# Kernel tuning notes

Measured on AMD Instinct MI355X. Metric: run time of the kernel, lower is better.

Reference implementation:

```python
import jax, jax.numpy as jnp
import numpy as np

E = 128      # n_routed_experts (hardcoded in DS_CONFIG_FOR_NEMOTRON)
I = 1856     # moe_intermediate_size
K = 6        # num_experts_per_tok
H = 512      # config.hidden_size
T = 4096     # flattened tokens (batch*seq)
C = 320      # per-expert capacity; avg load = T*K/E = 192, C=320 makes drops ~impossible


def setup_inputs() -> dict:
    key = jax.random.key(0)
    k1, k2, k3, k4, k5 = jax.random.split(key, 5)
    return {
        "hidden_states": jax.random.normal(k1, (T, H), jnp.float32),
        "top_k_index": jax.random.randint(k2, (T, K), 0, E, jnp.int32),
        "top_k_weights": jax.random.uniform(k3, (T, K), jnp.float32),
        "w_gate_up": jax.random.normal(k4, (E, H, 2 * I), jnp.float32) * 0.02,
        "w_down": jax.random.normal(k5, (E, I, H), jnp.float32) * 0.02,
    }


def reference(hidden_states, top_k_index, top_k_weights, w_gate_up, w_down):
    # Grouped-GEMM formulation of the naive per-expert loop: sort the (token, k)
    # pairs by expert, pack each expert's tokens into a fixed-capacity buffer,
    # run batched gate/up/down GEMMs over all experts at once, then weighted
    # scatter-add back to token order. Same math as the torch loop.
    N = T * K
    e = top_k_index.reshape(N)                      # expert id per pair
    tok = jnp.repeat(jnp.arange(T), K)              # token id per pair
    w = top_k_weights.reshape(N)

    order = jnp.argsort(e)                          # stable sort by expert
    e_s, tok_s, w_s = e[order], tok[order], w[order]

    counts = jax.ops.segment_sum(jnp.ones((N,), jnp.int32), e, num_segments=E)
    starts = jnp.cumsum(counts) - counts            # exclusive prefix sum
    pos = jnp.arange(N) - starts[e_s]               # rank within expert
    valid = pos < C                                 # capacity guard (never trips at this load)
    slot = jnp.where(valid, e_s * C + pos, E * C)   # overflow -> dummy slot

    # Dispatch: [E*C+1, H] buffer of gathered token states (dummy row absorbs overflow)
    buf = jnp.zeros((E * C + 1, H), hidden_states.dtype).at[slot].set(hidden_states[tok_s])
    x = buf[: E * C].reshape(E, C, H)

    gu = jnp.einsum('ech,ehf->ecf', x, w_gate_up)   # [E, C, 2I]
    gate, up = jnp.split(gu, 2, axis=-1)
    inter = jax.nn.silu(gate) * up                  # [E, C, I]
    y = jnp.einsum('eci,eih->ech', inter, w_down).reshape(E * C, H)

    # Combine: gather each pair's expert output, scale by router weight, scatter-add by token
    gather_idx = jnp.where(valid, e_s * C + pos, 0)
    pair_y = y[gather_idx] * jnp.where(valid, w_s, 0.0)[:, None]
    out = jnp.zeros((T, H), hidden_states.dtype).at[tok_s].add(pair_y)
    # use_context_proj=False: context states alias the hidden states
    return (out, out)
```

## Files before the change

### kernel.cpp

```cpp
#include <hip/hip_runtime.h>
#include <hip/hip_bf16.h>
#include <stdint.h>

#define NE 128
#define NI 1856
#define NKK 6
#define NH 512
#define NT 4096
#define CAP 320
#define NPAIR (NT*NKK)
#define LD2I (2*NI)

typedef unsigned short u16;
typedef __attribute__((ext_vector_type(4))) float f32x4;
typedef __attribute__((ext_vector_type(8))) short bf16x8;
typedef __attribute__((ext_vector_type(4))) short s16x4;
typedef const void __attribute__((address_space(1)))* gas1p;
typedef void __attribute__((address_space(3)))* gas3p;

__device__ __forceinline__ short f2bf(float f) {
  union { __hip_bfloat16 h; short s; } c; c.h = __float2bfloat16(f); return c.s;
}
__device__ __forceinline__ float bf2f(short s) {
  union { float f; unsigned u; } v; v.u = ((unsigned)(u16)s) << 16; return v.f;
}

__device__ __forceinline__ int xcd_logical(int bid, int n) {
  int q = n >> 3, r = n & 7;
  int xcd = bid & 7, j = bid >> 3;
  return xcd * q + (xcd < r ? xcd : r) + j;
}

__global__ void k_route(const int* __restrict__ topk, int* __restrict__ counts,
                        int* __restrict__ slot_of_pair, int* __restrict__ pair_of_slot) {
  int n = blockIdx.x * 256 + threadIdx.x;
  if (n >= NPAIR) return;
  int e = topk[n];
  int p = atomicAdd(&counts[e], 1);
  int s = (p < CAP) ? e * CAP + p : -1;
  slot_of_pair[n] = s;
  if (s >= 0) pair_of_slot[s] = n;
}

__global__ void k_gather(const float* __restrict__ hid, const int* __restrict__ counts,
                         const int* __restrict__ pair_of_slot, u16* __restrict__ xbuf) {
  int t = threadIdx.x;
  int row = blockIdx.x * 2 + (t >> 7);
  int c = t & 127;
  int e = row / CAP, p = row % CAP;
  if (p >= counts[e]) return;
  int n = pair_of_slot[row];
  int tok = n / NKK;
  f32x4 v = *(const f32x4*)(hid + (size_t)tok * NH + c * 4);
  s16x4 o;
  o[0] = f2bf(v[0]); o[1] = f2bf(v[1]); o[2] = f2bf(v[2]); o[3] = f2bf(v[3]);
  *(s16x4*)(xbuf + (size_t)row * NH + c * 4) = o;
}

__global__ __launch_bounds__(256, 3) void k_gemm1(
    const u16* __restrict__ xbuf, const float* __restrict__ wgu,
    const int* __restrict__ counts, u16* __restrict__ inter, int e0, int nblk)
{
  __shared__ __align__(16) char lds[40960];
  int L = xcd_logical(blockIdx.x, nblk);
  int el = L / 58, nt = L % 58;
  int e = e0 + el;
  int cnt = counts[e]; if (cnt > CAP) cnt = CAP;
  int n0 = nt * 32;
  int t = threadIdx.x, w = t >> 6, l = t & 63;
  int wm = w >> 1, wc = w & 1;
  const char* abase = (const char*)(xbuf + (size_t)e * CAP * NH);

  int bc = t & 63, bkc = t >> 6;
  int gcol = (bc < 32) ? (n0 + bc) : (NI + n0 + (bc - 32));
  const float* bsrc = wgu + (size_t)e * NH * LD2I + gcol;
  float bv[8];

  int kg16 = (l >> 4) * 16;
  int bcol0 = wc * 16 + (l & 15);
  int bswz = ((bcol0 & 3) << 4);

  for (int base = 0; base < cnt; base += 256) {
    __syncthreads();

    auto stageA = [&](int buf, int kt) {
      char* dstb = lds + buf * 16384;
      #pragma unroll
      for (int i = 0; i < 4; ++i) {
        int seg = i * 4 + w;
        int o = seg * 1024 + l * 16;
        int r = o >> 6, slot = o & 63;
        int grow = base + r; if (grow > CAP - 1) grow = CAP - 1;
        const char* g = abase + (size_t)grow * (NH * 2) + kt * 64 + (slot ^ ((r & 3) << 4));
        __builtin_amdgcn_global_load_lds((gas1p)g, (gas3p)(dstb + seg * 1024), 16, 0, 0);
      }
    };
    auto loadB = [&](int kt) {
      const float* p = bsrc + (size_t)(kt * 32 + bkc * 8) * LD2I;
      #pragma unroll
      for (int j = 0; j < 8; ++j) bv[j] = p[(size_t)j * LD2I];
    };
    auto writeB = [&](int buf) {
      bf16x8 o;
      #pragma unroll
      for (int j = 0; j < 8; ++j) o[j] = f2bf(bv[j]);
      char* bb = lds + 32768 + buf * 4096;
      *(bf16x8*)(bb + bc * 64 + ((bkc * 16) ^ ((bc & 3) << 4))) = o;
    };

    f32x4 acc[2][4][2];
    #pragma unroll
    for (int m = 0; m < 2; ++m)
      #pragma unroll
      for (int f = 0; f < 4; ++f) { acc[m][f][0] = (f32x4){0,0,0,0}; acc[m][f][1] = (f32x4){0,0,0,0}; }

    loadB(0);
    stageA(0, 0);
    writeB(0);

    for (int kt = 0; kt < 16; ++kt) {
      __syncthreads();
      int cur = kt & 1, nxt = cur ^ 1;
      if (kt + 1 < 16) { loadB(kt + 1); stageA(nxt, kt + 1); }
      const char* ab = lds + cur * 16384;
      const char* bb = lds + 32768 + cur * 4096;
      bf16x8 bg = *(const bf16x8*)(bb + bcol0 * 64 + (kg16 ^ bswz));
      bf16x8 bu = *(const bf16x8*)(bb + (32 + bcol0) * 64 + (kg16 ^ bswz));
      #pragma unroll
      for (int mt = 0; mt < 2; ++mt)
        #pragma unroll
        for (int mf = 0; mf < 4; ++mf) {
          int r = mt * 128 + wm * 64 + mf * 16 + (l & 15);
          bf16x8 af = *(const bf16x8*)(ab + r * 64 + (kg16 ^ ((r & 3) << 4)));
          acc[mt][mf][0] = __builtin_amdgcn_mfma_f32_16x16x32_bf16(af, bg, acc[mt][mf][0], 0, 0, 0);
          acc[mt][mf][1] = __builtin_amdgcn_mfma_f32_16x16x32_bf16(af, bu, acc[mt][mf][1], 0, 0, 0);
        }
      if (kt + 1 < 16) writeB(nxt);
    }

    __syncthreads();

    int cl = wc * 16 + (l & 15);
    #pragma unroll
    for (int mt = 0; mt < 2; ++mt)
      #pragma unroll
      for (int mf = 0; mf < 4; ++mf) {
        f32x4 g = acc[mt][mf][0], u = acc[mt][mf][1];
        #pragma unroll
        for (int r = 0; r < 4; ++r) {
          float gv = g[r];
          float val = gv / (1.f + __expf(-gv)) * u[r];
          int rl = mt * 128 + wm * 64 + mf * 16 + (l >> 4) * 4 + r;
          *(short*)(lds + rl * 64 + ((cl * 2) ^ ((rl & 3) << 4))) = f2bf(val);
        }
      }
    __syncthreads();
    int rmax = cnt - base; if (rmax > 256) rmax = 256;
    u16* obase = inter + (size_t)(el * CAP + base) * NI + n0;
    #pragma unroll
    for (int i = 0; i < 4; ++i) {
      int task = i * 256 + t;
      int r = task >> 2, p = task & 3;
      if (r < rmax) {
        bf16x8 v = *(const bf16x8*)(lds + r * 64 + ((p * 16) ^ ((r & 3) << 4)));
        *(bf16x8*)(obase + (size_t)r * NI + p * 8) = v;
      }
    }
  }
}

__global__ __launch_bounds__(256, 3) void k_gemm2(
    const u16* __restrict__ inter, const float* __restrict__ wdn,
    const int* __restrict__ counts, u16* __restrict__ Y, int e0, int nblk)
{
  __shared__ __align__(16) char lds[40960];
  int L = xcd_logical(blockIdx.x, nblk);
  int el = L / 8, nt = L % 8;
  int e = e0 + el;
  int cnt = counts[e]; if (cnt > CAP) cnt = CAP;
  int n0 = nt * 64;
  int t = threadIdx.x, w = t >> 6, l = t & 63;
  int wm = w >> 1, wc = w & 1;
  const char* abase = (const char*)(inter + (size_t)el * CAP * NI);

  int bc = t & 63, bkc = t >> 6;
  const float* bsrc = wdn + (size_t)e * NI * NH + n0 + bc;
  float bv[8];

  int kg16 = (l >> 4) * 16;
  int bcol0 = wc * 32 + (l & 15);
  int bswz = ((bcol0 & 3) << 4);

  for (int base = 0; base < cnt; base += 256) {
    __syncthreads();

    auto stageA = [&](int buf, int kt) {
      char* dstb = lds + buf * 16384;
      #pragma unroll
      for (int i = 0; i < 4; ++i) {
        int seg = i * 4 + w;
        int o = seg * 1024 + l * 16;
        int r = o >> 6, slot = o & 63;
        int grow = base + r; if (grow > CAP - 1) grow = CAP - 1;
        const char* g = abase + (size_t)grow * (NI * 2) + kt * 64 + (slot ^ ((r & 3) << 4));
        __builtin_amdgcn_global_load_lds((gas1p)g, (gas3p)(dstb + seg * 1024), 16, 0, 0);
      }
    };
    auto loadB = [&](int kt) {
      const float* p = bsrc + (size_t)(kt * 32 + bkc * 8) * NH;
      #pragma unroll
      for (int j = 0; j < 8; ++j) bv[j] = p[(size_t)j * NH];
    };
    auto writeB = [&](int buf) {
      bf16x8 o;
      #pragma unroll
      for (int j = 0; j < 8; ++j) o[j] = f2bf(bv[j]);
      char* bb = lds + 32768 + buf * 4096;
      *(bf16x8*)(bb + bc * 64 + ((bkc * 16) ^ ((bc & 3) << 4))) = o;
    };

    f32x4 acc[2][4][2];
    #pragma unroll
    for (int m = 0; m < 2; ++m)
      #pragma unroll
      for (int f = 0; f < 4; ++f) { acc[m][f][0] = (f32x4){0,0,0,0}; acc[m][f][1] = (f32x4){0,0,0,0}; }

    loadB(0);
    stageA(0, 0);
    writeB(0);

    for (int kt = 0; kt < 58; ++kt) {
      __syncthreads();
      int cur = kt & 1, nxt = cur ^ 1;
      if (kt + 1 < 58) { loadB(kt + 1); stageA(nxt, kt + 1); }
      const char* ab = lds + cur * 16384;
      const char* bb = lds + 32768 + cur * 4096;
      bf16x8 b0 = *(const bf16x8*)(bb + bcol0 * 64 + (kg16 ^ bswz));
      bf16x8 b1 = *(const bf16x8*)(bb + (16 + bcol0) * 64 + (kg16 ^ bswz));
      #pragma unroll
      for (int mt = 0; mt < 2; ++mt)
        #pragma unroll
        for (int mf = 0; mf < 4; ++mf) {
          int r = mt * 128 + wm * 64 + mf * 16 + (l & 15);
          bf16x8 af = *(const bf16x8*)(ab + r * 64 + (kg16 ^ ((r & 3) << 4)));
          acc[mt][mf][0] = __builtin_amdgcn_mfma_f32_16x16x32_bf16(af, b0, acc[mt][mf][0], 0, 0, 0);
          acc[mt][mf][1] = __builtin_amdgcn_mfma_f32_16x16x32_bf16(af, b1, acc[mt][mf][1], 0, 0, 0);
        }
      if (kt + 1 < 58) writeB(nxt);
    }

    __syncthreads();

    #pragma unroll
    for (int mt = 0; mt < 2; ++mt)
      #pragma unroll
      for (int mf = 0; mf < 4; ++mf)
        #pragma unroll
        for (int f = 0; f < 2; ++f) {
          f32x4 a = acc[mt][mf][f];
          int cl = wc * 32 + f * 16 + (l & 15);
          #pragma unroll
          for (int r = 0; r < 4; ++r) {
            int rl = mt * 128 + wm * 64 + mf * 16 + (l >> 4) * 4 + r;
            *(short*)(lds + rl * 128 + ((cl * 2) ^ ((rl & 7) << 4))) = f2bf(a[r]);
          }
        }
    __syncthreads();
    int rmax = cnt - base; if (rmax > 256) rmax = 256;
    u16* obase = Y + (size_t)(e * CAP + base) * NH + n0;
    #pragma unroll
    for (int i = 0; i < 8; ++i) {
      int task = i * 256 + t;
      int r = task >> 3, p = task & 7;
      if (r < rmax) {
        bf16x8 v = *(const bf16x8*)(lds + r * 128 + ((p * 16) ^ ((r & 7) << 4)));
        *(bf16x8*)(obase + (size_t)r * NH + p * 8) = v;
      }
    }
  }
}

__global__ void k_combine(const int* __restrict__ slot_of_pair, const float* __restrict__ wts,
                          const u16* __restrict__ Y, float* __restrict__ out)
{
  int t = threadIdx.x;
  int tok = blockIdx.x * 2 + (t >> 7);
  int c = t & 127;
  f32x4 a = (f32x4){0.f, 0.f, 0.f, 0.f};
  #pragma unroll
  for (int k = 0; k < NKK; ++k) {
    int n = tok * NKK + k;
    int s = slot_of_pair[n];
    if (s >= 0) {
      float wv = wts[n];
      s16x4 y = *(const s16x4*)(Y + (size_t)s * NH + c * 4);
      a[0] += wv * bf2f(y[0]);
      a[1] += wv * bf2f(y[1]);
      a[2] += wv * bf2f(y[2]);
      a[3] += wv * bf2f(y[3]);
    }
  }
  *(f32x4*)(out + (size_t)tok * NH + c * 4) = a;
  *(f32x4*)(out + (size_t)(NT + tok) * NH + c * 4) = a;
}

extern "C" void kernel_launch(void* const* d_in, const int* in_sizes, int n_in,
                              void* d_out, int out_size, void* d_ws, size_t ws_size,
                              hipStream_t stream) {
  const float* hid  = (const float*)d_in[0];
  const int*   topk = (const int*)d_in[1];
  const float* wts  = (const float*)d_in[2];
  const float* wgu  = (const float*)d_in[3];
  const float* wdn  = (const float*)d_in[4];

  char* ws = (char*)d_ws;
  size_t off = 0;
  auto alloc = [&](size_t sz) { char* p = ws + off; off = (off + sz + 255) & ~(size_t)255; return p; };
  int* counts        = (int*)alloc(NE * 4);
  int* slot_of_pair  = (int*)alloc((size_t)NPAIR * 4);
  int* pair_of_slot  = (int*)alloc((size_t)NE * CAP * 4);
  u16* xbuf          = (u16*)alloc((size_t)NE * CAP * NH * 2);
  u16* Y             = (u16*)alloc((size_t)NE * CAP * NH * 2);
  size_t remain = ws_size > off ? ws_size - off : 0;
  size_t per_e = (size_t)CAP * NI * 2;
  int chunkE = (int)(remain / per_e);
  if (chunkE > NE) chunkE = NE;
  if (chunkE < 1) chunkE = 1;
  u16* inter = (u16*)(ws + off);

  hipMemsetAsync(counts, 0, NE * 4, stream);
  k_route<<<NPAIR / 256, 256, 0, stream>>>(topk, counts, slot_of_pair, pair_of_slot);
  k_gather<<<NE * CAP / 2, 256, 0, stream>>>(hid, counts, pair_of_slot, xbuf);
  for (int e0 = 0; e0 < NE; e0 += chunkE) {
    int ce = NE - e0 < chunkE ? NE - e0 : chunkE;
    int nb1 = ce * 58;
    int nb2 = ce * 8;
    k_gemm1<<<nb1, 256, 0, stream>>>(xbuf, wgu, counts, inter, e0, nb1);
    k_gemm2<<<nb2, 256, 0, stream>>>(inter, wdn, counts, Y, e0, nb2);
  }
  k_combine<<<NT / 2, 256, 0, stream>>>(slot_of_pair, wts, Y, (float*)d_out);
}
```

Measured before the change: 642.5 us.

## Stage fp32 weights via async LDS loads with triple-buffered pipeline

Both GEMM kernels now copy the fp32 weight tiles straight into LDS with global_load_lds, where the old code loaded them into registers, converted to bf16 and wrote them back. The conversion to bf16 moves to the LDS read side. The K-loop becomes a 3-stage ring buffer with explicit vmcnt waits and raw s_barrier, which keeps two tiles in flight and removes the register round-trip for B. This grows LDS to 72KB and drops occupancy from 3 to 2 blocks per CU. It also adds scalar fp32 LDS reads plus conversions in the inner loop, which may cause bank conflicts.

```diff
diff --git a/kernel.cpp b/kernel.cpp
--- a/kernel.cpp
+++ b/kernel.cpp
@@ -17,6 +17,8 @@
 typedef __attribute__((ext_vector_type(4))) short s16x4;
 typedef const void __attribute__((address_space(1)))* gas1p;
 typedef void __attribute__((address_space(3)))* gas3p;
+
+#define SFENCE __builtin_amdgcn_sched_barrier(0)
 
 __device__ __forceinline__ short f2bf(float f) {
   union { __hip_bfloat16 h; short s; } c; c.h = __float2bfloat16(f); return c.s;
@@ -57,11 +59,11 @@
   *(s16x4*)(xbuf + (size_t)row * NH + c * 4) = o;
 }
 
-__global__ __launch_bounds__(256, 3) void k_gemm1(
+__global__ __launch_bounds__(256, 2) void k_gemm1(
     const u16* __restrict__ xbuf, const float* __restrict__ wgu,
     const int* __restrict__ counts, u16* __restrict__ inter, int e0, int nblk)
 {
-  __shared__ __align__(16) char lds[40960];
+  __shared__ __align__(16) char lds[73728];
   int L = xcd_logical(blockIdx.x, nblk);
   int el = L / 58, nt = L % 58;
   int e = e0 + el;
@@ -71,20 +73,20 @@
   int wm = w >> 1, wc = w & 1;
   const char* abase = (const char*)(xbuf + (size_t)e * CAP * NH);
 
-  int bc = t & 63, bkc = t >> 6;
-  int gcol = (bc < 32) ? (n0 + bc) : (NI + n0 + (bc - 32));
+  int bks = l >> 4;
+  int c4 = (l & 15) * 4;
+  int gcol = (c4 < 32) ? (n0 + c4) : (NI + n0 + (c4 - 32));
   const float* bsrc = wgu + (size_t)e * NH * LD2I + gcol;
-  float bv[8];
-
-  int kg16 = (l >> 4) * 16;
-  int bcol0 = wc * 16 + (l & 15);
-  int bswz = ((bcol0 & 3) << 4);
+
+  int kg = l >> 4;
+  int kg16 = kg * 16;
+  int colg = wc * 16 + (l & 15);
 
   for (int base = 0; base < cnt; base += 256) {
     __syncthreads();
 
-    auto stageA = [&](int buf, int kt) {
-      char* dstb = lds + buf * 16384;
+    auto STAGE = [&](int buf, int kt) {
+      char* ad = lds + buf * 16384;
       #pragma unroll
       for (int i = 0; i < 4; ++i) {
         int seg = i * 4 + w;
@@ -92,21 +94,17 @@
         int r = o >> 6, slot = o & 63;
         int grow = base + r; if (grow > CAP - 1) grow = CAP - 1;
         const char* g = abase + (size_t)grow * (NH * 2) + kt * 64 + (slot ^ ((r & 3) << 4));
-        __builtin_amdgcn_global_load_lds((gas1p)g, (gas3p)(dstb + seg * 1024), 16, 0, 0);
+        __builtin_amdgcn_global_load_lds((gas1p)g, (gas3p)(ad + seg * 1024), 16, 0, 0);
+      }
+      char* bd = lds + 49152 + buf * 8192;
+      #pragma unroll
+      for (int i = 0; i < 2; ++i) {
+        int seg = w * 2 + i;
+        int k = seg * 4 + bks;
+        const char* g = (const char*)(bsrc + (size_t)(kt * 32 + k) * LD2I);
+        __builtin_amdgcn_global_load_lds((gas1p)g, (gas3p)(bd + seg * 1024), 16, 0, 0);
       }
     };
-    auto loadB = [&](int kt) {
-      const float* p = bsrc + (size_t)(kt * 32 + bkc * 8) * LD2I;
-      #pragma unroll
-      for (int j = 0; j < 8; ++j) bv[j] = p[(size_t)j * LD2I];
-    };
-    auto writeB = [&](int buf) {
-      bf16x8 o;
-      #pragma unroll
-      for (int j = 0; j < 8; ++j) o[j] = f2bf(bv[j]);
-      char* bb = lds + 32768 + buf * 4096;
-      *(bf16x8*)(bb + bc * 64 + ((bkc * 16) ^ ((bc & 3) << 4))) = o;
-    };
 
     f32x4 acc[2][4][2];
     #pragma unroll
@@ -114,18 +112,24 @@
       #pragma unroll
       for (int f = 0; f < 4; ++f) { acc[m][f][0] = (f32x4){0,0,0,0}; acc[m][f][1] = (f32x4){0,0,0,0}; }
 
-    loadB(0);
-    stageA(0, 0);
-    writeB(0);
+    STAGE(0, 0);
+    STAGE(1, 1);
+    SFENCE; asm volatile("s_waitcnt vmcnt(6) lgkmcnt(0)" ::: "memory"); SFENCE;
 
     for (int kt = 0; kt < 16; ++kt) {
-      __syncthreads();
-      int cur = kt & 1, nxt = cur ^ 1;
-      if (kt + 1 < 16) { loadB(kt + 1); stageA(nxt, kt + 1); }
-      const char* ab = lds + cur * 16384;
-      const char* bb = lds + 32768 + cur * 4096;
-      bf16x8 bg = *(const bf16x8*)(bb + bcol0 * 64 + (kg16 ^ bswz));
-      bf16x8 bu = *(const bf16x8*)(bb + (32 + bcol0) * 64 + (kg16 ^ bswz));
+      SFENCE; __builtin_amdgcn_s_barrier(); SFENCE;
+      int sk = (kt + 2 < 16) ? kt + 2 : 15;
+      STAGE((kt + 2) % 3, sk);
+
+      const char* ab = lds + (kt % 3) * 16384;
+      const char* bb = lds + 49152 + (kt % 3) * 8192;
+      bf16x8 bg, bu;
+      #pragma unroll
+      for (int j = 0; j < 8; ++j) {
+        int k = kg * 8 + j;
+        bg[j] = f2bf(*(const float*)(bb + k * 256 + colg * 4));
+        bu[j] = f2bf(*(const float*)(bb + k * 256 + (colg + 32) * 4));
+      }
       #pragma unroll
       for (int mt = 0; mt < 2; ++mt)
         #pragma unroll
@@ -135,9 +139,8 @@
           acc[mt][mf][0] = __builtin_amdgcn_mfma_f32_16x16x32_bf16(af, bg, acc[mt][mf][0], 0, 0, 0);
           acc[mt][mf][1] = __builtin_amdgcn_mfma_f32_16x16x32_bf16(af, bu, acc[mt][mf][1], 0, 0, 0);
         }
-      if (kt + 1 < 16) writeB(nxt);
-    }
-
+      SFENCE; asm volatile("s_waitcnt vmcnt(6) lgkmcnt(0)" ::: "memory"); SFENCE;
+    }
     __syncthreads();
 
     int cl = wc * 16 + (l & 15);
@@ -169,11 +172,11 @@
   }
 }
 
-__global__ __launch_bounds__(256, 3) void k_gemm2(
+__global__ __launch_bounds__(256, 2) void k_gemm2(
     const u16* __restrict__ inter, const float* __restrict__ wdn,
     const int* __restrict__ counts, u16* __restrict__ Y, int e0, int nblk)
 {
-  __shared__ __align__(16) char lds[40960];
+  __shared__ __align__(16) char lds[73728];
   int L = xcd_logical(blockIdx.x, nblk);
   int el = L / 8, nt = L % 8;
   int e = e0 + el;
@@ -183,19 +186,19 @@
   int wm = w >> 1, wc = w & 1;
   const char* abase = (const char*)(inter + (size_t)el * CAP * NI);
 
-  int bc = t & 63, bkc = t >> 6;
-  const float* bsrc = wdn + (size_t)e * NI * NH + n0 + bc;
-  float bv[8];
-
-  int kg16 = (l >> 4) * 16;
-  int bcol0 = wc * 32 + (l & 15);
-  int bswz = ((bcol0 & 3) << 4);
+  int bks = l >> 4;
+  int c4 = (l & 15) * 4;
+  const float* bsrc = wdn + (size_t)e * NI * NH + n0 + c4;
+
+  int kg = l >> 4;
+  int kg16 = kg * 16;
+  int col0 = wc * 32 + (l & 15);
 
   for (int base = 0; base < cnt; base += 256) {
     __syncthreads();
 
-    auto stageA = [&](int buf, int kt) {
-      char* dstb = lds + buf * 16384;
+    auto STAGE = [&](int buf, int kt) {
+      char* ad = lds + buf * 16384;
       #pragma unroll
       for (int i = 0; i < 4; ++i) {
         int seg = i * 4 + w;
@@ -203,21 +206,17 @@
         int r = o >> 6, slot = o & 63;
         int grow = base + r; if (grow > CAP - 1) grow = CAP - 1;
         const char* g = abase + (size_t)grow * (NI * 2) + kt * 64 + (slot ^ ((r & 3) << 4));
-        __builtin_amdgcn_global_load_lds((gas1p)g, (gas3p)(dstb + seg * 1024), 16, 0, 0);
+        __builtin_amdgcn_global_load_lds((gas1p)g, (gas3p)(ad + seg * 1024), 16, 0, 0);
+      }
+      char* bd = lds + 49152 + buf * 8192;
+      #pragma unroll
+      for (int i = 0; i < 2; ++i) {
+        int seg = w * 2 + i;
+        int k = seg * 4 + bks;
+        const char* g = (const char*)(bsrc + (size_t)(kt * 32 + k) * NH);
+        __builtin_amdgcn_global_load_lds((gas1p)g, (gas3p)(bd + seg * 1024), 16, 0, 0);
       }
     };
-    auto loadB = [&](int kt) {
-      const float* p = bsrc + (size_t)(kt * 32 + bkc * 8) * NH;
-      #pragma unroll
-      for (int j = 0; j < 8; ++j) bv[j] = p[(size_t)j * NH];
-    };
-    auto writeB = [&](int buf) {
-      bf16x8 o;
-      #pragma unroll
-      for (int j = 0; j < 8; ++j) o[j] = f2bf(bv[j]);
-      char* bb = lds + 32768 + buf * 4096;
-      *(bf16x8*)(bb + bc * 64 + ((bkc * 16) ^ ((bc & 3) << 4))) = o;
-    };
 
     f32x4 acc[2][4][2];
     #pragma unroll
@@ -225,18 +224,24 @@
       #pragma unroll
       for (int f = 0; f < 4; ++f) { acc[m][f][0] = (f32x4){0,0,0,0}; acc[m][f][1] = (f32x4){0,0,0,0}; }
 
-    loadB(0);
-    stageA(0, 0);
-    writeB(0);
+    STAGE(0, 0);
+    STAGE(1, 1);
+    SFENCE; asm volatile("s_waitcnt vmcnt(6) lgkmcnt(0)" ::: "memory"); SFENCE;
 
     for (int kt = 0; kt < 58; ++kt) {
-      __syncthreads();
-      int cur = kt & 1, nxt = cur ^ 1;
-      if (kt + 1 < 58) { loadB(kt + 1); stageA(nxt, kt + 1); }
-      const char* ab = lds + cur * 16384;
-      const char* bb = lds + 32768 + cur * 4096;
-      bf16x8 b0 = *(const bf16x8*)(bb + bcol0 * 64 + (kg16 ^ bswz));
-      bf16x8 b1 = *(const bf16x8*)(bb + (16 + bcol0) * 64 + (kg16 ^ bswz));
+      SFENCE; __builtin_amdgcn_s_barrier(); SFENCE;
+      int sk = (kt + 2 < 58) ? kt + 2 : 57;
+      STAGE((kt + 2) % 3, sk);
+
+      const char* ab = lds + (kt % 3) * 16384;
+      const char* bb = lds + 49152 + (kt % 3) * 8192;
+      bf16x8 b0, b1;
+      #pragma unroll
+      for (int j = 0; j < 8; ++j) {
+        int k = kg * 8 + j;
+        b0[j] = f2bf(*(const float*)(bb + k * 256 + col0 * 4));
+        b1[j] = f2bf(*(const float*)(bb + k * 256 + (col0 + 16) * 4));
+      }
       #pragma unroll
       for (int mt = 0; mt < 2; ++mt)
         #pragma unroll
@@ -246,9 +251,8 @@
           acc[mt][mf][0] = __builtin_amdgcn_mfma_f32_16x16x32_bf16(af, b0, acc[mt][mf][0], 0, 0, 0);
           acc[mt][mf][1] = __builtin_amdgcn_mfma_f32_16x16x32_bf16(af, b1, acc[mt][mf][1], 0, 0, 0);
         }
-      if (kt + 1 < 58) writeB(nxt);
-    }
-
+      SFENCE; asm volatile("s_waitcnt vmcnt(6) lgkmcnt(0)" ::: "memory"); SFENCE;
+    }
     __syncthreads();
 
     #pragma unroll
```

Measured after the change: 534.5 us. -16.8%, faster.
